# Performance work log

Hardware: AMD Instinct MI355X
Metric: run time of the kernel (lower is better)

Reference implementation:

```python
import jax, jax.numpy as jnp
import numpy as np


def gcn_layer(h, src, dst, norm, W, b, num_nodes):
    # PyG GCNConv: linear transform, normalized scatter-add aggregation, then bias
    h = h @ W                                    # [N, out]
    msg = h[src] * norm[:, None]                 # [E+N, out] gathered messages
    out = jax.ops.segment_sum(msg, dst, num_segments=num_nodes)
    return out + b


def setup_inputs() -> dict:
    key = jax.random.key(0)
    ks = jax.random.split(key, 6)
    N, E, D, H, C = 100000, 1600000, 128, 64, 2
    x = jax.random.normal(ks[0], (N, D), dtype=jnp.float32)
    edge_index = jax.random.randint(ks[1], (2, E), 0, N, dtype=jnp.int64)
    def glorot(k, shape):
        lim = np.sqrt(6.0 / (shape[0] + shape[1]))
        return jax.random.uniform(k, shape, jnp.float32, -lim, lim)
    return {
        "x": x,
        "edge_index": edge_index,
        "W1": glorot(ks[2], (D, H)), "b1": jnp.zeros((H,), jnp.float32),
        "W2": glorot(ks[3], (H, H)), "b2": jnp.zeros((H,), jnp.float32),
        "W3": glorot(ks[4], (H, H)), "b3": jnp.zeros((H,), jnp.float32),
        "Wfc": glorot(ks[5], (H, C)), "bfc": jnp.zeros((C,), jnp.float32),
    }


def reference(x, edge_index, W1, b1, W2, b2, W3, b3, Wfc, bfc):
    N = x.shape[0]
    # add self loops (GCNConv default), symmetric deg^-1/2 normalization
    loops = jnp.arange(N, dtype=edge_index.dtype)
    src = jnp.concatenate([edge_index[0], loops])
    dst = jnp.concatenate([edge_index[1], loops])
    deg = jax.ops.segment_sum(jnp.ones_like(dst, dtype=x.dtype), dst, num_segments=N)
    dinv = jnp.where(deg > 0, jax.lax.rsqrt(deg), 0.0)
    norm = dinv[src] * dinv[dst]

    h = jax.nn.relu(gcn_layer(x, src, dst, norm, W1, b1, N))
    h = jax.nn.relu(gcn_layer(h, src, dst, norm, W2, b2, N))
    h = jax.nn.relu(gcn_layer(h, src, dst, norm, W3, b3, N))
    logits = h @ Wfc + bfc
    return jax.nn.log_softmax(logits, axis=1)
```

## Files before the change

### kernel.cpp

```cpp
#include <hip/hip_runtime.h>
#include <math.h>


static inline size_t alignup(size_t x){ return (x + 511) & ~size_t(511); }

typedef float v4f __attribute__((ext_vector_type(4)));
typedef unsigned short v4u16 __attribute__((ext_vector_type(4)));
typedef __attribute__((ext_vector_type(8))) short short8;
typedef __attribute__((ext_vector_type(4))) float f32x4;

__device__ __forceinline__ unsigned short f32_to_bf16(float f){
  union { float f; unsigned int u; } c; c.f = f;
  unsigned int u = c.u + 0x7FFFu + ((c.u >> 16) & 1u);
  return (unsigned short)(u >> 16);
}
__device__ __forceinline__ v4f bf16x4_to_f32(v4u16 a){
  union { unsigned int u; float f; } c0,c1,c2,c3;
  c0.u = (unsigned int)a.x << 16;
  c1.u = (unsigned int)a.y << 16;
  c2.u = (unsigned int)a.z << 16;
  c3.u = (unsigned int)a.w << 16;
  v4f r; r.x=c0.f; r.y=c1.f; r.z=c2.f; r.w=c3.f;
  return r;
}

#define NBUCK 1024
#define CHUNK 8192
#define CCAP  3584

__device__ __forceinline__ void wfrag_one(const float* __restrict__ W,
                                          unsigned short* __restrict__ wf,
                                          int idx, int ksteps){
  int total = ksteps*4*64;
  if(idx >= total) return;
  int l  = idx & 63;
  int nb = (idx>>6) & 3;
  int ks = idx>>8;
  int k0 = ks*32 + 8*(l>>4);
  int n  = nb*16 + (l&15);
  unsigned short* o = wf + (size_t)idx*8;
  #pragma unroll
  for(int i=0;i<8;i++) o[i] = f32_to_bf16(W[(size_t)(k0+i)*64 + n]);
}

__global__ __launch_bounds__(256) void setup_kernel(const float* __restrict__ W1,
                                                    const float* __restrict__ W2,
                                                    const float* __restrict__ W3,
                                                    unsigned short* __restrict__ wf1,
                                                    unsigned short* __restrict__ wf2,
                                                    unsigned short* __restrict__ wf3,
                                                    int* __restrict__ bfill,
                                                    unsigned short* __restrict__ gAz,
                                                    unsigned short* __restrict__ gBz){
  int b = blockIdx.x, t = threadIdx.x;
  if(b < 4)      wfrag_one(W1, wf1, b*256+t, 4);
  else if(b < 6) wfrag_one(W2, wf2, (b-4)*256+t, 2);
  else           wfrag_one(W3, wf3, (b-6)*256+t, 2);
  if(b < 4) bfill[b*256+t] = 0;
  if(b==4 && t<32) ((int*)gAz)[t] = 0;
  if(b==5 && t<32) ((int*)gBz)[t] = 0;
}

__global__ __launch_bounds__(1024) void scatter_kernel(const int* __restrict__ src,
                                                       const int* __restrict__ dst,
                                                       int* __restrict__ bfill,
                                                       int* __restrict__ pairs, int E){
  __shared__ int hist[NBUCK];
  __shared__ int delta[NBUCK];
  __shared__ int wsum[16];
  __shared__ int vals[CHUNK];
  __shared__ unsigned short bkt[CHUNK];
  int t = threadIdx.x;
  int lane = t & 63, wid = t >> 6;
  int cbase = blockIdx.x*CHUNK;
  hist[t]=0;
  __syncthreads();
  #pragma unroll
  for(int i=0;i<CHUNK;i+=1024){
    int e = cbase+i+t;
    if(e<E) atomicAdd(&hist[dst[e]>>7], 1);
  }
  __syncthreads();
  int v = hist[t];
  int x = v;
  #pragma unroll
  for(int off=1; off<64; off<<=1){
    int y = __shfl_up(x, off, 64);
    if(lane >= off) x += y;
  }
  if(lane==63) wsum[wid]=x;
  __syncthreads();
  if(wid==0){
    int s2 = (lane<16) ? wsum[lane] : 0;
    #pragma unroll
    for(int off=1; off<16; off<<=1){
      int y = __shfl_up(s2, off, 64);
      if(lane >= off) s2 += y;
    }
    if(lane<16) wsum[lane]=s2;
  }
  __syncthreads();
  int run = (x - v) + (wid ? wsum[wid-1] : 0);
  int g = v ? atomicAdd(&bfill[t], v) : 0;
  hist[t]=run; delta[t]= t*CCAP + g - run;
  __syncthreads();
  #pragma unroll
  for(int i=0;i<CHUNK;i+=1024){
    int e = cbase+i+t;
    if(e<E){
      int d = dst[e];
      int b = d>>7;
      int slot = atomicAdd(&hist[b], 1);
      vals[slot] = ((d&127)<<17) | src[e];
      bkt[slot]  = (unsigned short)b;
    }
  }
  __syncthreads();
  int cnt = E - cbase; if(cnt > CHUNK) cnt = CHUNK;
  for(int i=t;i<cnt;i+=1024){
    int b = bkt[i];
    pairs[delta[b] + i] = vals[i];
  }
}

__global__ __launch_bounds__(256) void bucket_csr_kernel(const int* __restrict__ pairs,
                                                         const int* __restrict__ bfill,
                                                         int2* __restrict__ rowse,
                                                         float* __restrict__ dinv,
                                                         int* __restrict__ col,
                                                         int N){
  __shared__ int hist[128];
  __shared__ int pref[128];
  __shared__ int fill[128];
  __shared__ int srcs[CCAP];
  int b = blockIdx.x, t = threadIdx.x;
  int s0 = b*CCAP;
  int cnt = bfill[b]; if(cnt > CCAP) cnt = CCAP;
  if(t<128) hist[t]=0;
  __syncthreads();
  int v[CCAP/256];
  #pragma unroll
  for(int i=0;i<CCAP/256;i++){
    int idx = i*256 + t;
    if(idx<cnt){ v[i]=pairs[s0+idx]; atomicAdd(&hist[v[i]>>17], 1); }
  }
  __syncthreads();
  if(t<128) pref[t]=hist[t];
  __syncthreads();
  for(int off=1; off<128; off<<=1){
    int x=0;
    if(t<128 && t>=off) x=pref[t-off];
    __syncthreads();
    if(t<128) pref[t]+=x;
    __syncthreads();
  }
  if(t<128){
    int ex = pref[t]-hist[t];
    fill[t]=ex;
    int node = b*128 + t;
    if(node<N){
      rowse[node] = make_int2(s0+ex, s0+ex+hist[t]);
      dinv[node] = rsqrtf((float)(hist[t]+1));
    }
  }
  __syncthreads();
  #pragma unroll
  for(int i=0;i<CCAP/256;i++){
    int idx = i*256 + t;
    if(idx<cnt){
      int ld = v[i]>>17;
      int pos = atomicAdd(&fill[ld], 1);
      srcs[pos] = v[i] & 0x1FFFF;
    }
  }
  __syncthreads();
  for(int i=t;i<cnt;i+=256) col[s0+i]=srcs[i];
}

__global__ __launch_bounds__(256) void lin_mfma_kernel(const float* __restrict__ x,
                                                       const unsigned short* __restrict__ wf,
                                                       const float* __restrict__ dinv,
                                                       unsigned short* __restrict__ g,
                                                       int N){
  __shared__ __align__(16) unsigned short wl[4*4*64*8];
  int t = threadIdx.x, wave = t>>6, lane = t&63;
  #pragma unroll
  for(int idx=t; idx<1024; idx+=256)
    ((v4f*)wl)[idx] = ((const v4f*)wf)[idx];
  __syncthreads();
  int row = blockIdx.x*64 + wave*16 + (lane&15);
  int arow = row < N ? row : N-1;
  const float* xr = x + (size_t)arow*128 + 8*(lane>>4);
  f32x4 acc0={0.f,0.f,0.f,0.f}, acc1=acc0, acc2=acc0, acc3=acc0;
  #pragma unroll
  for(int ks=0; ks<4; ks++){
    v4f a0 = *(const v4f*)(xr + ks*32);
    v4f a1 = *(const v4f*)(xr + ks*32 + 4);
    short8 af;
    af[0]=(short)f32_to_bf16(a0.x); af[1]=(short)f32_to_bf16(a0.y);
    af[2]=(short)f32_to_bf16(a0.z); af[3]=(short)f32_to_bf16(a0.w);
    af[4]=(short)f32_to_bf16(a1.x); af[5]=(short)f32_to_bf16(a1.y);
    af[6]=(short)f32_to_bf16(a1.z); af[7]=(short)f32_to_bf16(a1.w);
    const short8* wb = ((const short8*)wl) + ks*256 + lane;
    acc0 = __builtin_amdgcn_mfma_f32_16x16x32_bf16(af, wb[0],   acc0, 0, 0, 0);
    acc1 = __builtin_amdgcn_mfma_f32_16x16x32_bf16(af, wb[64],  acc1, 0, 0, 0);
    acc2 = __builtin_amdgcn_mfma_f32_16x16x32_bf16(af, wb[128], acc2, 0, 0, 0);
    acc3 = __builtin_amdgcn_mfma_f32_16x16x32_bf16(af, wb[192], acc3, 0, 0, 0);
  }
  int rbase = blockIdx.x*64 + wave*16 + (lane>>4)*4;
  int c = lane & 15;
  #pragma unroll
  for(int j=0;j<4;j++){
    int r = rbase + j;
    if(r < N){
      float dv = dinv[r];
      unsigned short* go = g + (size_t)r*64 + c;
      go[0]  = f32_to_bf16(dv*acc0[j]);
      go[16] = f32_to_bf16(dv*acc1[j]);
      go[32] = f32_to_bf16(dv*acc2[j]);
      go[48] = f32_to_bf16(dv*acc3[j]);
    }
  }
}

__device__ __forceinline__ v4f gather_row4(const unsigned short* __restrict__ g,
                                           const int* __restrict__ col,
                                           int n, int s, int e, int l, int ZR){
  v4f acc = bf16x4_to_f32(*(const v4u16*)&g[(size_t)n*64 + l*4]);
  for(int i = s; i < e; i += 16){
    int rem = e - i;
    int myc = (l < rem) ? col[i + l] : ZR;
    #pragma unroll
    for(int j0 = 0; j0 < 16; j0 += 4){
      int c0 = __shfl(myc, j0+0, 16);
      int c1 = __shfl(myc, j0+1, 16);
      int c2 = __shfl(myc, j0+2, 16);
      int c3 = __shfl(myc, j0+3, 16);
      v4f x0 = bf16x4_to_f32(*(const v4u16*)&g[(size_t)c0*64 + l*4]);
      v4f x1 = bf16x4_to_f32(*(const v4u16*)&g[(size_t)c1*64 + l*4]);
      v4f x2 = bf16x4_to_f32(*(const v4u16*)&g[(size_t)c2*64 + l*4]);
      v4f x3 = bf16x4_to_f32(*(const v4u16*)&g[(size_t)c3*64 + l*4]);
      acc = acc + ((x0 + x1) + (x2 + x3));
      if(j0+4 >= rem) break;
    }
  }
  return acc;
}

__global__ __launch_bounds__(256) void agg_lin_kernel(const unsigned short* __restrict__ g,
                                                      const int2* __restrict__ rowse,
                                                      const int* __restrict__ col,
                                                      const float* __restrict__ dinv,
                                                      const float* __restrict__ bias,
                                                      const unsigned short* __restrict__ wf,
                                                      unsigned short* __restrict__ g2,
                                                      int N){
  __shared__ __align__(16) unsigned short hsh[16*72];
  __shared__ __align__(16) unsigned short wl[2*4*64*8];
  int t = threadIdx.x, wave = t>>6, lane = t&63;
  int l = lane & 15, q = lane >> 4;
  #pragma unroll
  for(int idx = t; idx < 512; idx += 256)
    ((v4f*)wl)[idx] = ((const v4f*)wf)[idx];
  int base = blockIdx.x*16;
  int n = base + wave*4 + q;
  bool valid = n < N;
  int nn = valid ? n : (N-1);
  int2 se = rowse[nn];
  v4f acc = gather_row4(g, col, nn, se.x, se.y, l, N);
  float dv = dinv[nn];
  v4f bs = *(const v4f*)&bias[l*4];
  v4u16 hb;
  hb.x = f32_to_bf16(fmaxf(fmaf(dv, acc.x, bs.x), 0.f));
  hb.y = f32_to_bf16(fmaxf(fmaf(dv, acc.y, bs.y), 0.f));
  hb.z = f32_to_bf16(fmaxf(fmaf(dv, acc.z, bs.z), 0.f));
  hb.w = f32_to_bf16(fmaxf(fmaf(dv, acc.w, bs.w), 0.f));
  *(v4u16*)&hsh[(wave*4+q)*72 + l*4] = hb;
  __syncthreads();
  short8 a0 = *(const short8*)&hsh[(lane&15)*72 +      8*(lane>>4)];
  short8 a1 = *(const short8*)&hsh[(lane&15)*72 + 32 + 8*(lane>>4)];
  const short8* wb = ((const short8*)wl) + wave*64 + lane;
  f32x4 oc = {0.f,0.f,0.f,0.f};
  oc = __builtin_amdgcn_mfma_f32_16x16x32_bf16(a0, wb[0],   oc, 0, 0, 0);
  oc = __builtin_amdgcn_mfma_f32_16x16x32_bf16(a1, wb[256], oc, 0, 0, 0);
  int c  = wave*16 + (lane&15);
  int r0 = base + (lane>>4)*4;
  #pragma unroll
  for(int j=0;j<4;j++){
    int r = r0 + j;
    if(r < N)
      g2[(size_t)r*64 + c] = f32_to_bf16(dinv[r]*oc[j]);
  }
}

__global__ __launch_bounds__(256) void agg_final_kernel(const unsigned short* __restrict__ g,
                                                        const int2* __restrict__ rowse,
                                                        const int* __restrict__ col,
                                                        const float* __restrict__ dinv,
                                                        const float* __restrict__ bias,
                                                        const float* __restrict__ Wfc,
                                                        const float* __restrict__ bfc,
                                                        float* __restrict__ out, int N){
  int t = threadIdx.x, wave = t>>6, lane = t&63;
  int l = lane & 15, q = lane >> 4;
  int n = blockIdx.x*16 + wave*4 + q;
  bool valid = n < N;
  if(!valid) n = N-1;
  int2 se = rowse[n];
  v4f acc = gather_row4(g, col, n, se.x, se.y, l, N);
  float dv = dinv[n];
  v4f bs = *(const v4f*)&bias[l*4];
  v4f hv;
  hv.x = fmaxf(fmaf(dv, acc.x, bs.x), 0.f);
  hv.y = fmaxf(fmaf(dv, acc.y, bs.y), 0.f);
  hv.z = fmaxf(fmaf(dv, acc.z, bs.z), 0.f);
  hv.w = fmaxf(fmaf(dv, acc.w, bs.w), 0.f);
  v4f wa = *(const v4f*)&Wfc[l*8];
  v4f wb = *(const v4f*)&Wfc[l*8+4];
  float p0 = hv.x*wa.x + hv.y*wa.z + hv.z*wb.x + hv.w*wb.z;
  float p1 = hv.x*wa.y + hv.y*wa.w + hv.z*wb.y + hv.w*wb.w;
  for(int off=8; off; off>>=1){
    p0 += __shfl_down(p0, off, 16);
    p1 += __shfl_down(p1, off, 16);
  }
  if(valid && l==0){
    float l0 = p0 + bfc[0], l1 = p1 + bfc[1];
    float m  = fmaxf(l0, l1);
    float lse = m + logf(expf(l0-m) + expf(l1-m));
    out[(size_t)n*2+0] = l0 - lse;
    out[(size_t)n*2+1] = l1 - lse;
  }
}

extern "C" void kernel_launch(void* const* d_in, const int* in_sizes, int n_in,
                              void* d_out, int out_size, void* d_ws, size_t ws_size,
                              hipStream_t stream) {
  (void)n_in; (void)out_size; (void)ws_size;
  const float* x   = (const float*)d_in[0];
  const int*   ei  = (const int*)  d_in[1];
  const float* W1  = (const float*)d_in[2];
  const float* b1  = (const float*)d_in[3];
  const float* W2  = (const float*)d_in[4];
  const float* b2  = (const float*)d_in[5];
  const float* W3  = (const float*)d_in[6];
  const float* b3  = (const float*)d_in[7];
  const float* Wfc = (const float*)d_in[8];
  const float* bfc = (const float*)d_in[9];
  float* out = (float*)d_out;

  const int N = in_sizes[0] / 128;
  const int E = in_sizes[1] / 2;
  const int* src = ei;
  const int* dst = ei + E;
  const int NB = (N + 127) / 128;

  char* w = (char*)d_ws;
  int*   bfill   = (int*)  w; w += alignup((size_t)NBUCK*4);
  int*   pairs   = (int*)  w; w += alignup((size_t)NBUCK*CCAP*4);
  int2*  rowse   = (int2*) w; w += alignup((size_t)N*8);
  float* dinv    = (float*)w; w += alignup((size_t)N*4);
  int*   col     = (int*)  w; w += alignup((size_t)NBUCK*CCAP*4);
  unsigned short* gA = (unsigned short*)w; w += alignup((size_t)(N+1)*64*2);
  unsigned short* gB = (unsigned short*)w; w += alignup((size_t)(N+1)*64*2);
  unsigned short* wf1 = (unsigned short*)w; w += alignup((size_t)4*4*64*8*2);
  unsigned short* wf2 = (unsigned short*)w; w += alignup((size_t)2*4*64*8*2);
  unsigned short* wf3 = (unsigned short*)w; w += alignup((size_t)2*4*64*8*2);

  const int nblkE   = (E + CHUNK - 1) / CHUNK;
  const int nblkLin = (N + 63) / 64;
  const int nblkAgg = (N + 15) / 16;

  setup_kernel<<<8, 256, 0, stream>>>(W1, W2, W3, wf1, wf2, wf3, bfill,
                                      gA + (size_t)N*64, gB + (size_t)N*64);
  scatter_kernel<<<nblkE, 1024, 0, stream>>>(src, dst, bfill, pairs, E);
  bucket_csr_kernel<<<NB, 256, 0, stream>>>(pairs, bfill, rowse, dinv, col, N);

  lin_mfma_kernel<<<nblkLin, 256, 0, stream>>>(x, wf1, dinv, gA, N);
  agg_lin_kernel<<<nblkAgg, 256, 0, stream>>>(gA, rowse, col, dinv, b1, wf2, gB, N);
  agg_lin_kernel<<<nblkAgg, 256, 0, stream>>>(gB, rowse, col, dinv, b2, wf3, gA, N);
  agg_final_kernel<<<nblkAgg, 256, 0, stream>>>(gA, rowse, col, dinv, b3,
                                                Wfc, bfc, out, N);
}
```

Measured before the change: 234.6 us.

## Gather rows with 8 lanes and 16-byte loads, 8 nodes per wave

The aggregation gather now gives each node 8 lanes that each load 16 bytes (8 bf16 values) instead of 16 lanes loading 8 bytes. Each wave therefore covers 8 nodes and each block 32, so the fused MFMA epilogue is reorganised: each wave computes two 16-column tiles for one of two 16-row tiles. The aim is wider memory transactions and more independent gathers in flight per wave. In exchange each lane holds more registers, and column indices are fetched in batches of 8 rather than 16.

```diff
diff --git a/kernel.cpp b/kernel.cpp
--- a/kernel.cpp
+++ b/kernel.cpp
@@ -6,6 +6,7 @@
 
 typedef float v4f __attribute__((ext_vector_type(4)));
 typedef unsigned short v4u16 __attribute__((ext_vector_type(4)));
+typedef unsigned short v8u16 __attribute__((ext_vector_type(8)));
 typedef __attribute__((ext_vector_type(8))) short short8;
 typedef __attribute__((ext_vector_type(4))) float f32x4;
 
@@ -22,6 +23,12 @@
   c3.u = (unsigned int)a.w << 16;
   v4f r; r.x=c0.f; r.y=c1.f; r.z=c2.f; r.w=c3.f;
   return r;
+}
+__device__ __forceinline__ v4f bf16lo(v8u16 r){
+  v4u16 t; t.x=r[0]; t.y=r[1]; t.z=r[2]; t.w=r[3]; return bf16x4_to_f32(t);
+}
+__device__ __forceinline__ v4f bf16hi(v8u16 r){
+  v4u16 t; t.x=r[4]; t.y=r[5]; t.z=r[6]; t.w=r[7]; return bf16x4_to_f32(t);
 }
 
 #define NBUCK 1024
@@ -223,28 +230,30 @@
   }
 }
 
-__device__ __forceinline__ v4f gather_row4(const unsigned short* __restrict__ g,
-                                           const int* __restrict__ col,
-                                           int n, int s, int e, int l, int ZR){
-  v4f acc = bf16x4_to_f32(*(const v4u16*)&g[(size_t)n*64 + l*4]);
-  for(int i = s; i < e; i += 16){
+__device__ __forceinline__ void gather_row8(const unsigned short* __restrict__ g,
+                                            const int* __restrict__ col,
+                                            int n, int s, int e, int l, int ZR,
+                                            v4f& accA, v4f& accB){
+  v8u16 sr = *(const v8u16*)&g[(size_t)n*64 + l*8];
+  accA = bf16lo(sr); accB = bf16hi(sr);
+  for(int i = s; i < e; i += 8){
     int rem = e - i;
     int myc = (l < rem) ? col[i + l] : ZR;
     #pragma unroll
-    for(int j0 = 0; j0 < 16; j0 += 4){
-      int c0 = __shfl(myc, j0+0, 16);
-      int c1 = __shfl(myc, j0+1, 16);
-      int c2 = __shfl(myc, j0+2, 16);
-      int c3 = __shfl(myc, j0+3, 16);
-      v4f x0 = bf16x4_to_f32(*(const v4u16*)&g[(size_t)c0*64 + l*4]);
-      v4f x1 = bf16x4_to_f32(*(const v4u16*)&g[(size_t)c1*64 + l*4]);
-      v4f x2 = bf16x4_to_f32(*(const v4u16*)&g[(size_t)c2*64 + l*4]);
-      v4f x3 = bf16x4_to_f32(*(const v4u16*)&g[(size_t)c3*64 + l*4]);
-      acc = acc + ((x0 + x1) + (x2 + x3));
+    for(int j0 = 0; j0 < 8; j0 += 4){
+      int c0 = __shfl(myc, j0+0, 8);
+      int c1 = __shfl(myc, j0+1, 8);
+      int c2 = __shfl(myc, j0+2, 8);
+      int c3 = __shfl(myc, j0+3, 8);
+      v8u16 x0 = *(const v8u16*)&g[(size_t)c0*64 + l*8];
+      v8u16 x1 = *(const v8u16*)&g[(size_t)c1*64 + l*8];
+      v8u16 x2 = *(const v8u16*)&g[(size_t)c2*64 + l*8];
+      v8u16 x3 = *(const v8u16*)&g[(size_t)c3*64 + l*8];
+      accA = accA + ((bf16lo(x0) + bf16lo(x1)) + (bf16lo(x2) + bf16lo(x3)));
+      accB = accB + ((bf16hi(x0) + bf16hi(x1)) + (bf16hi(x2) + bf16hi(x3)));
       if(j0+4 >= rem) break;
     }
   }
-  return acc;
 }
 
 __global__ __launch_bounds__(256) void agg_lin_kernel(const unsigned short* __restrict__ g,
@@ -255,41 +264,55 @@
                                                       const unsigned short* __restrict__ wf,
                                                       unsigned short* __restrict__ g2,
                                                       int N){
-  __shared__ __align__(16) unsigned short hsh[16*72];
+  __shared__ __align__(16) unsigned short hsh[32*72];
   __shared__ __align__(16) unsigned short wl[2*4*64*8];
   int t = threadIdx.x, wave = t>>6, lane = t&63;
-  int l = lane & 15, q = lane >> 4;
+  int l = lane & 7, q = lane >> 3;
   #pragma unroll
   for(int idx = t; idx < 512; idx += 256)
     ((v4f*)wl)[idx] = ((const v4f*)wf)[idx];
-  int base = blockIdx.x*16;
-  int n = base + wave*4 + q;
+  int base = blockIdx.x*32;
+  int n = base + wave*8 + q;
   bool valid = n < N;
   int nn = valid ? n : (N-1);
   int2 se = rowse[nn];
-  v4f acc = gather_row4(g, col, nn, se.x, se.y, l, N);
+  v4f aA, aB;
+  gather_row8(g, col, nn, se.x, se.y, l, N, aA, aB);
   float dv = dinv[nn];
-  v4f bs = *(const v4f*)&bias[l*4];
-  v4u16 hb;
-  hb.x = f32_to_bf16(fmaxf(fmaf(dv, acc.x, bs.x), 0.f));
-  hb.y = f32_to_bf16(fmaxf(fmaf(dv, acc.y, bs.y), 0.f));
-  hb.z = f32_to_bf16(fmaxf(fmaf(dv, acc.z, bs.z), 0.f));
-  hb.w = f32_to_bf16(fmaxf(fmaf(dv, acc.w, bs.w), 0.f));
-  *(v4u16*)&hsh[(wave*4+q)*72 + l*4] = hb;
-  __syncthreads();
-  short8 a0 = *(const short8*)&hsh[(lane&15)*72 +      8*(lane>>4)];
-  short8 a1 = *(const short8*)&hsh[(lane&15)*72 + 32 + 8*(lane>>4)];
-  const short8* wb = ((const short8*)wl) + wave*64 + lane;
-  f32x4 oc = {0.f,0.f,0.f,0.f};
-  oc = __builtin_amdgcn_mfma_f32_16x16x32_bf16(a0, wb[0],   oc, 0, 0, 0);
-  oc = __builtin_amdgcn_mfma_f32_16x16x32_bf16(a1, wb[256], oc, 0, 0, 0);
-  int c  = wave*16 + (lane&15);
-  int r0 = base + (lane>>4)*4;
+  v4f b0 = *(const v4f*)&bias[l*8];
+  v4f b1 = *(const v4f*)&bias[l*8+4];
+  v8u16 hb;
+  hb[0] = f32_to_bf16(fmaxf(fmaf(dv, aA.x, b0.x), 0.f));
+  hb[1] = f32_to_bf16(fmaxf(fmaf(dv, aA.y, b0.y), 0.f));
+  hb[2] = f32_to_bf16(fmaxf(fmaf(dv, aA.z, b0.z), 0.f));
+  hb[3] = f32_to_bf16(fmaxf(fmaf(dv, aA.w, b0.w), 0.f));
+  hb[4] = f32_to_bf16(fmaxf(fmaf(dv, aB.x, b1.x), 0.f));
+  hb[5] = f32_to_bf16(fmaxf(fmaf(dv, aB.y, b1.y), 0.f));
+  hb[6] = f32_to_bf16(fmaxf(fmaf(dv, aB.z, b1.z), 0.f));
+  hb[7] = f32_to_bf16(fmaxf(fmaf(dv, aB.w, b1.w), 0.f));
+  *(v8u16*)&hsh[(wave*8+q)*72 + l*8] = hb;
+  __syncthreads();
+  int rt = wave >> 1;
+  int cb = (wave & 1)*2;
+  const unsigned short* hrow = &hsh[(rt*16 + (lane&15))*72 + 8*(lane>>4)];
+  short8 a0 = *(const short8*)hrow;
+  short8 a1 = *(const short8*)(hrow + 32);
+  const short8* wbp = (const short8*)wl;
+  f32x4 oc0 = {0.f,0.f,0.f,0.f}, oc1 = oc0;
+  oc0 = __builtin_amdgcn_mfma_f32_16x16x32_bf16(a0, wbp[      cb*64 + lane], oc0, 0, 0, 0);
+  oc0 = __builtin_amdgcn_mfma_f32_16x16x32_bf16(a1, wbp[256 + cb*64 + lane], oc0, 0, 0, 0);
+  oc1 = __builtin_amdgcn_mfma_f32_16x16x32_bf16(a0, wbp[      (cb+1)*64 + lane], oc1, 0, 0, 0);
+  oc1 = __builtin_amdgcn_mfma_f32_16x16x32_bf16(a1, wbp[256 + (cb+1)*64 + lane], oc1, 0, 0, 0);
+  int c  = cb*16 + (lane&15);
+  int r0 = base + rt*16 + (lane>>4)*4;
   #pragma unroll
   for(int j=0;j<4;j++){
     int r = r0 + j;
-    if(r < N)
-      g2[(size_t)r*64 + c] = f32_to_bf16(dinv[r]*oc[j]);
+    if(r < N){
+      float dv2 = dinv[r];
+      g2[(size_t)r*64 + c]      = f32_to_bf16(dv2*oc0[j]);
+      g2[(size_t)r*64 + c + 16] = f32_to_bf16(dv2*oc1[j]);
+    }
   }
 }
 
@@ -302,26 +325,36 @@
                                                         const float* __restrict__ bfc,
                                                         float* __restrict__ out, int N){
   int t = threadIdx.x, wave = t>>6, lane = t&63;
-  int l = lane & 15, q = lane >> 4;
-  int n = blockIdx.x*16 + wave*4 + q;
+  int l = lane & 7, q = lane >> 3;
+  int n = blockIdx.x*32 + wave*8 + q;
   bool valid = n < N;
   if(!valid) n = N-1;
   int2 se = rowse[n];
-  v4f acc = gather_row4(g, col, n, se.x, se.y, l, N);
+  v4f aA, aB;
+  gather_row8(g, col, n, se.x, se.y, l, N, aA, aB);
   float dv = dinv[n];
-  v4f bs = *(const v4f*)&bias[l*4];
-  v4f hv;
-  hv.x = fmaxf(fmaf(dv, acc.x, bs.x), 0.f);
-  hv.y = fmaxf(fmaf(dv, acc.y, bs.y), 0.f);
-  hv.z = fmaxf(fmaf(dv, acc.z, bs.z), 0.f);
-  hv.w = fmaxf(fmaf(dv, acc.w, bs.w), 0.f);
-  v4f wa = *(const v4f*)&Wfc[l*8];
-  v4f wb = *(const v4f*)&Wfc[l*8+4];
-  float p0 = hv.x*wa.x + hv.y*wa.z + hv.z*wb.x + hv.w*wb.z;
-  float p1 = hv.x*wa.y + hv.y*wa.w + hv.z*wb.y + hv.w*wb.w;
-  for(int off=8; off; off>>=1){
-    p0 += __shfl_down(p0, off, 16);
-    p1 += __shfl_down(p1, off, 16);
+  v4f b0 = *(const v4f*)&bias[l*8];
+  v4f b1 = *(const v4f*)&bias[l*8+4];
+  v4f hA, hB;
+  hA.x = fmaxf(fmaf(dv, aA.x, b0.x), 0.f);
+  hA.y = fmaxf(fmaf(dv, aA.y, b0.y), 0.f);
+  hA.z = fmaxf(fmaf(dv, aA.z, b0.z), 0.f);
+  hA.w = fmaxf(fmaf(dv, aA.w, b0.w), 0.f);
+  hB.x = fmaxf(fmaf(dv, aB.x, b1.x), 0.f);
+  hB.y = fmaxf(fmaf(dv, aB.y, b1.y), 0.f);
+  hB.z = fmaxf(fmaf(dv, aB.z, b1.z), 0.f);
+  hB.w = fmaxf(fmaf(dv, aB.w, b1.w), 0.f);
+  v4f wa = *(const v4f*)&Wfc[l*16];
+  v4f wb = *(const v4f*)&Wfc[l*16+4];
+  v4f wc = *(const v4f*)&Wfc[l*16+8];
+  v4f wd = *(const v4f*)&Wfc[l*16+12];
+  float p0 = hA.x*wa.x + hA.y*wa.z + hA.z*wb.x + hA.w*wb.z
+           + hB.x*wc.x + hB.y*wc.z + hB.z*wd.x + hB.w*wd.z;
+  float p1 = hA.x*wa.y + hA.y*wa.w + hA.z*wb.y + hA.w*wb.w
+           + hB.x*wc.y + hB.y*wc.w + hB.z*wd.y + hB.w*wd.w;
+  for(int off=4; off; off>>=1){
+    p0 += __shfl_down(p0, off, 8);
+    p1 += __shfl_down(p1, off, 8);
   }
   if(valid && l==0){
     float l0 = p0 + bfc[0], l1 = p1 + bfc[1];
@@ -368,7 +401,7 @@
 
   const int nblkE   = (E + CHUNK - 1) / CHUNK;
   const int nblkLin = (N + 63) / 64;
-  const int nblkAgg = (N + 15) / 16;
+  const int nblkAgg = (N + 31) / 32;
 
   setup_kernel<<<8, 256, 0, stream>>>(W1, W2, W3, wf1, wf2, wf3, bfill,
                                       gA + (size_t)N*64, gB + (size_t)N*64);
```

Measured after the change: 238.1 us. Within noise of the previous version (+1.5%).

## Sort nodes by degree within each bucket to balance aggregation warps

Applied to the files above, without the earlier changes.

The CSR build now counting-sorts the nodes of each 128-node bucket by in-degree and writes a permutation array. The aggregation kernels process nodes in that permuted order, so the 16-lane groups sharing a wave handle nodes of similar degree and wait less on divergent gather loops. Outputs are scattered back through the permutation. This costs an extra scan in bucket_csr, an extra indirection per node, and less contiguous writes of g2.

```diff
diff --git a/kernel.cpp b/kernel.cpp
--- a/kernel.cpp
+++ b/kernel.cpp
@@ -128,15 +128,18 @@
                                                          int2* __restrict__ rowse,
                                                          float* __restrict__ dinv,
                                                          int* __restrict__ col,
+                                                         int* __restrict__ perm,
                                                          int N){
   __shared__ int hist[128];
   __shared__ int pref[128];
   __shared__ int fill[128];
+  __shared__ int dh[128];
+  __shared__ int dp[128];
   __shared__ int srcs[CCAP];
   int b = blockIdx.x, t = threadIdx.x;
   int s0 = b*CCAP;
   int cnt = bfill[b]; if(cnt > CCAP) cnt = CCAP;
-  if(t<128) hist[t]=0;
+  if(t<128){ hist[t]=0; dh[t]=0; }
   __syncthreads();
   int v[CCAP/256];
   #pragma unroll
@@ -154,14 +157,33 @@
     if(t<128) pref[t]+=x;
     __syncthreads();
   }
+  int node = b*128 + t;
+  int degc = 0;
   if(t<128){
     int ex = pref[t]-hist[t];
     fill[t]=ex;
-    int node = b*128 + t;
     if(node<N){
       rowse[node] = make_int2(s0+ex, s0+ex+hist[t]);
       dinv[node] = rsqrtf((float)(hist[t]+1));
-    }
+      degc = hist[t] < 127 ? hist[t] : 127;
+      atomicAdd(&dh[degc], 1);
+    }
+  }
+  __syncthreads();
+  if(t<128) dp[t]=dh[t];
+  __syncthreads();
+  for(int off=1; off<128; off<<=1){
+    int x=0;
+    if(t<128 && t>=off) x=dp[t-off];
+    __syncthreads();
+    if(t<128) dp[t]+=x;
+    __syncthreads();
+  }
+  if(t<128) dh[t] = dp[t]-dh[t];
+  __syncthreads();
+  if(t<128 && node<N){
+    int r = atomicAdd(&dh[degc], 1);
+    perm[b*128 + r] = node;
   }
   __syncthreads();
   #pragma unroll
@@ -253,6 +275,7 @@
                                                       const float* __restrict__ dinv,
                                                       const float* __restrict__ bias,
                                                       const unsigned short* __restrict__ wf,
+                                                      const int* __restrict__ perm,
                                                       unsigned short* __restrict__ g2,
                                                       int N){
   __shared__ __align__(16) unsigned short hsh[16*72];
@@ -263,12 +286,11 @@
   for(int idx = t; idx < 512; idx += 256)
     ((v4f*)wl)[idx] = ((const v4f*)wf)[idx];
   int base = blockIdx.x*16;
-  int n = base + wave*4 + q;
-  bool valid = n < N;
-  int nn = valid ? n : (N-1);
-  int2 se = rowse[nn];
-  v4f acc = gather_row4(g, col, nn, se.x, se.y, l, N);
-  float dv = dinv[nn];
+  int slot = base + wave*4 + q;
+  int n = perm[slot < N ? slot : N-1];
+  int2 se = rowse[n];
+  v4f acc = gather_row4(g, col, n, se.x, se.y, l, N);
+  float dv = dinv[n];
   v4f bs = *(const v4f*)&bias[l*4];
   v4u16 hb;
   hb.x = f32_to_bf16(fmaxf(fmaf(dv, acc.x, bs.x), 0.f));
@@ -288,8 +310,10 @@
   #pragma unroll
   for(int j=0;j<4;j++){
     int r = r0 + j;
-    if(r < N)
-      g2[(size_t)r*64 + c] = f32_to_bf16(dinv[r]*oc[j]);
+    if(r < N){
+      int pn = perm[r];
+      g2[(size_t)pn*64 + c] = f32_to_bf16(dinv[pn]*oc[j]);
+    }
   }
 }
 
@@ -300,12 +324,13 @@
                                                         const float* __restrict__ bias,
                                                         const float* __restrict__ Wfc,
                                                         const float* __restrict__ bfc,
+                                                        const int* __restrict__ perm,
                                                         float* __restrict__ out, int N){
   int t = threadIdx.x, wave = t>>6, lane = t&63;
   int l = lane & 15, q = lane >> 4;
-  int n = blockIdx.x*16 + wave*4 + q;
-  bool valid = n < N;
-  if(!valid) n = N-1;
+  int slot = blockIdx.x*16 + wave*4 + q;
+  bool valid = slot < N;
+  int n = perm[valid ? slot : N-1];
   int2 se = rowse[n];
   v4f acc = gather_row4(g, col, n, se.x, se.y, l, N);
   float dv = dinv[n];
@@ -359,6 +384,7 @@
   int*   pairs   = (int*)  w; w += alignup((size_t)NBUCK*CCAP*4);
   int2*  rowse   = (int2*) w; w += alignup((size_t)N*8);
   float* dinv    = (float*)w; w += alignup((size_t)N*4);
+  int*   perm    = (int*)  w; w += alignup((size_t)(N+16)*4);
   int*   col     = (int*)  w; w += alignup((size_t)NBUCK*CCAP*4);
   unsigned short* gA = (unsigned short*)w; w += alignup((size_t)(N+1)*64*2);
   unsigned short* gB = (unsigned short*)w; w += alignup((size_t)(N+1)*64*2);
@@ -373,11 +399,11 @@
   setup_kernel<<<8, 256, 0, stream>>>(W1, W2, W3, wf1, wf2, wf3, bfill,
                                       gA + (size_t)N*64, gB + (size_t)N*64);
   scatter_kernel<<<nblkE, 1024, 0, stream>>>(src, dst, bfill, pairs, E);
-  bucket_csr_kernel<<<NB, 256, 0, stream>>>(pairs, bfill, rowse, dinv, col, N);
+  bucket_csr_kernel<<<NB, 256, 0, stream>>>(pairs, bfill, rowse, dinv, col, perm, N);
 
   lin_mfma_kernel<<<nblkLin, 256, 0, stream>>>(x, wf1, dinv, gA, N);
-  agg_lin_kernel<<<nblkAgg, 256, 0, stream>>>(gA, rowse, col, dinv, b1, wf2, gB, N);
-  agg_lin_kernel<<<nblkAgg, 256, 0, stream>>>(gB, rowse, col, dinv, b2, wf3, gA, N);
+  agg_lin_kernel<<<nblkAgg, 256, 0, stream>>>(gA, rowse, col, dinv, b1, wf2, perm, gB, N);
+  agg_lin_kernel<<<nblkAgg, 256, 0, stream>>>(gB, rowse, col, dinv, b2, wf3, perm, gA, N);
   agg_final_kernel<<<nblkAgg, 256, 0, stream>>>(gA, rowse, col, dinv, b3,
-                                                Wfc, bfc, out, N);
-}
+                                                Wfc, bfc, perm, out, N);
+}
```

Result: slower. 263.5 us (+12.3%).
